# Kernel tuning notes

Measured on AMD Instinct MI355X. Metric: run time of the kernel, lower is better.

Reference implementation:

```python
import jax, jax.numpy as jnp
import numpy as np

W_BITS = 8
A_BITS = 8


def sym_quant(x, num_bits):
    # Symmetric per-last-dim abs-max quantization (SymQuantizer.forward, ndim<=3,
    # layerwise=False): s = (2^(b-1)-1)/(max|x| + 1e-6); q = round(x*s)/(s+1e-6)
    max_abs = jnp.max(jnp.abs(x), axis=-1, keepdims=True)
    s = (2.0 ** (num_bits - 1) - 1.0) / (max_abs + 1e-6)
    return jnp.round(x * s) / (s + 1e-6)


def setup_inputs() -> dict:
    key = jax.random.key(0)
    kx, kw = jax.random.split(key)
    B, S, NX, NF = 4, 2048, 1600, 6400
    x = jax.random.normal(kx, (B, S, NX), dtype=jnp.float32)
    weight = 0.02 * jax.random.normal(kw, (NX, NF), dtype=jnp.float32)  # Conv1D: [nx, nf]
    bias = jnp.zeros((NF,), dtype=jnp.float32)
    return {"x": x, "weight": weight, "bias": bias}


def reference(x, weight, bias):
    # quantize weights per-row (over nf), quantize activations per-token (over nx)
    wq = sym_quant(weight, W_BITS)
    xq = sym_quant(x, A_BITS)
    # addmm(bias, x.view(-1, nx), weight) then reshape back
    return jnp.einsum("bsx,xf->bsf", xq, wq) + bias
```

## Files before the change

### kernel.cpp

```cpp
#include <hip/hip_runtime.h>
#include <stdint.h>

typedef _Float16 f16;
typedef _Float16 f16x4 __attribute__((ext_vector_type(4)));
typedef _Float16 f16x8 __attribute__((ext_vector_type(8)));
typedef float f32x4 __attribute__((ext_vector_type(4)));

#define K_DIM 1600
#define NF_DIM 6400
#define KPAD 1664
#define NKT 26

__device__ __forceinline__ void async_copy16(const void* g, void* l) {
    __builtin_amdgcn_global_load_lds(
        (const __attribute__((address_space(1))) void*)(uintptr_t)g,
        (__attribute__((address_space(3))) void*)(uint32_t)(uintptr_t)l,
        16, 0, 0);
}

__device__ __forceinline__ float blockMax(float v, float* sm) {
#pragma unroll
    for (int off = 32; off > 0; off >>= 1)
        v = fmaxf(v, __shfl_down(v, off, 64));
    int wid = threadIdx.x >> 6, lane = threadIdx.x & 63;
    if (lane == 0) sm[wid] = v;
    __syncthreads();
    if (threadIdx.x == 0) {
        float m = sm[0];
        for (int i = 1; i < (int)(blockDim.x >> 6); ++i) m = fmaxf(m, sm[i]);
        sm[0] = m;
    }
    __syncthreads();
    return sm[0];
}

__global__ void quant_x_kernel(const float* __restrict__ x, f16* __restrict__ qx,
                               float* __restrict__ ax) {
    __shared__ float sm[4];
    size_t row = blockIdx.x;
    const float* xr = x + row * (size_t)K_DIM;
    float m = 0.f;
    const int n4 = K_DIM >> 2;
    for (int i = threadIdx.x; i < n4; i += blockDim.x) {
        float4 v = ((const float4*)xr)[i];
        m = fmaxf(fmaxf(fmaxf(fabsf(v.x), fabsf(v.y)), fmaxf(fabsf(v.z), fabsf(v.w))), m);
    }
    m = blockMax(m, sm);
    float s = 127.0f / (m + 1e-6f);
    if (threadIdx.x == 0) ax[row] = 1.0f / (s + 1e-6f);
    f16* qr = qx + row * (size_t)KPAD;
    for (int i = threadIdx.x; i < n4; i += blockDim.x) {
        float4 v = ((const float4*)xr)[i];
        f16x4 q;
        q[0] = (f16)rintf(v.x * s);
        q[1] = (f16)rintf(v.y * s);
        q[2] = (f16)rintf(v.z * s);
        q[3] = (f16)rintf(v.w * s);
        *(f16x4*)&qr[i * 4] = q;
    }
    if (threadIdx.x < 16) {
        f16x4 z = {};
        *(f16x4*)&qr[K_DIM + threadIdx.x * 4] = z;
    }
}

__global__ void wscale_kernel(const float* __restrict__ w, float* __restrict__ sw) {
    __shared__ float sm[4];
    size_t k = blockIdx.x;
    const float* wr = w + k * (size_t)NF_DIM;
    float m = 0.f;
    const int n4 = NF_DIM >> 2;
    for (int i = threadIdx.x; i < n4; i += blockDim.x) {
        float4 v = ((const float4*)wr)[i];
        m = fmaxf(fmaxf(fmaxf(fabsf(v.x), fabsf(v.y)), fmaxf(fabsf(v.z), fabsf(v.w))), m);
    }
    m = blockMax(m, sm);
    if (threadIdx.x == 0) sw[k] = 127.0f / (m + 1e-6f);
}

__global__ void wtq_kernel(const float* __restrict__ w, const float* __restrict__ sw,
                           f16* __restrict__ wqt) {
    __shared__ f16 t[64][80];
    int k0 = blockIdx.x * 64;
    int f0 = blockIdx.y * 64;
    int tid = threadIdx.x;
    if (k0 >= K_DIM) {
        int fr = tid >> 2;
        int ch = (tid & 3) << 4;
        float4 z = {};
        float4* dst = (float4*)&wqt[(size_t)(f0 + fr) * KPAD + k0 + ch];
        dst[0] = z;
        dst[1] = z;
        return;
    }
    int rr = tid >> 4;
    int cc = (tid & 15) << 2;
#pragma unroll
    for (int i = 0; i < 4; ++i) {
        int r = rr + i * 16;
        float s = sw[k0 + r];
        float inv = 1.0f / (s + 1e-6f);
        float4 v = *(const float4*)&w[(size_t)(k0 + r) * NF_DIM + f0 + cc];
        t[cc + 0][r] = (f16)(rintf(v.x * s) * inv);
        t[cc + 1][r] = (f16)(rintf(v.y * s) * inv);
        t[cc + 2][r] = (f16)(rintf(v.z * s) * inv);
        t[cc + 3][r] = (f16)(rintf(v.w * s) * inv);
    }
    __syncthreads();
    int fr = tid >> 2;
    int ch = (tid & 3) << 4;
    const float4* src = (const float4*)&t[fr][ch];
    float4* dst = (float4*)&wqt[(size_t)(f0 + fr) * KPAD + k0 + ch];
    dst[0] = src[0];
    dst[1] = src[1];
}

__global__ __launch_bounds__(512, 1) void gemm256(
    const f16* __restrict__ A,
    const f16* __restrict__ Bt,
    const float* __restrict__ ax,
    const float* __restrict__ bias,
    float* __restrict__ C, int M, int N) {
    extern __shared__ char lds[];

    const int tid = threadIdx.x;
    const int lane = tid & 63;
    const int wv = tid >> 6;
    const int wm = wv >> 2;
    const int wn = wv & 3;
    const int lr = lane & 15;
    const int lg = lane >> 4;

    const int nTn = N / 256;
    const int bid = blockIdx.x;
    const int cpx = gridDim.x >> 3;
    const int swz = (bid & 7) * cpx + (bid >> 3);
    const int tm = swz / nTn, tn = swz % nTn;
    const size_t m0 = (size_t)tm * 256, n0 = (size_t)tn * 256;

    const int srow8 = lane >> 3;
    const int sslot = (lane & 7) ^ srow8;

#define STAGE_HALF(mat, row0, kb, lhalf)                                              \
    {                                                                                 \
        _Pragma("unroll") for (int j = 0; j < 2; ++j) {                               \
            int L = (wv * 2 + j) * 1024 + lane * 16;                                  \
            int row = wv * 16 + j * 8 + srow8;                                        \
            const char* g = (const char*)((mat) + ((row0) + row) * (size_t)KPAD) +    \
                            (kb) + sslot * 16;                                        \
            async_copy16(g, (lhalf) + L);                                             \
        }                                                                             \
    }

#define STAGE_TILE(kidx, buf)                                   \
    {                                                           \
        int kb_ = (kidx) * 128;                                 \
        STAGE_HALF(A, m0, kb_, (buf));                          \
        STAGE_HALF(A, m0 + 128, kb_, (buf) + 16384);            \
        STAGE_HALF(Bt, n0, kb_, (buf) + 32768);                 \
        STAGE_HALF(Bt, n0 + 128, kb_, (buf) + 49152);           \
    }

#define LDF(base, row, s) \
    (*(const f16x8*)((base) + (row) * 128 + ((((s) ^ ((row) & 7))) << 4)))

    f32x4 acc[8][4] = {};

    STAGE_TILE(0, lds);
    STAGE_TILE(1, lds + 65536);
    asm volatile("s_waitcnt vmcnt(8)" ::: "memory");
    asm volatile("s_barrier" ::: "memory");

    for (int kt = 0; kt < NKT; ++kt) {
        char* buf = lds + (kt & 1) * 65536;
        const char* Ab = buf;
        const char* Bb = buf + 32768;
        int pf = (kt + 2 < NKT) ? kt + 2 : NKT - 1;

        f16x8 alo[4][2], ahi[4][2], bA[2][2], bB[2][2];

#pragma unroll
        for (int mi = 0; mi < 4; ++mi)
#pragma unroll
            for (int kk = 0; kk < 2; ++kk)
                alo[mi][kk] = LDF(Ab, wm * 128 + mi * 16 + lr, kk * 4 + lg);
#pragma unroll
        for (int ni = 0; ni < 2; ++ni)
#pragma unroll
            for (int kk = 0; kk < 2; ++kk)
                bA[ni][kk] = LDF(Bb, wn * 64 + ni * 16 + lr, kk * 4 + lg);
        asm volatile("s_barrier" ::: "memory");
        asm volatile("s_waitcnt lgkmcnt(0)" ::: "memory");
        __builtin_amdgcn_sched_barrier(0);
        __builtin_amdgcn_s_setprio(1);
#pragma unroll
        for (int mi = 0; mi < 4; ++mi)
#pragma unroll
            for (int ni = 0; ni < 2; ++ni)
#pragma unroll
                for (int kk = 0; kk < 2; ++kk)
                    acc[mi][ni] = __builtin_amdgcn_mfma_f32_16x16x32_f16(
                        alo[mi][kk], bA[ni][kk], acc[mi][ni], 0, 0, 0);
        __builtin_amdgcn_s_setprio(0);
        asm volatile("s_barrier" ::: "memory");

#pragma unroll
        for (int mi = 0; mi < 4; ++mi)
#pragma unroll
            for (int kk = 0; kk < 2; ++kk)
                ahi[mi][kk] = LDF(Ab, wm * 128 + 64 + mi * 16 + lr, kk * 4 + lg);
        asm volatile("s_barrier" ::: "memory");
        asm volatile("s_waitcnt lgkmcnt(0)" ::: "memory");
        __builtin_amdgcn_sched_barrier(0);
        __builtin_amdgcn_s_setprio(1);
#pragma unroll
        for (int mi = 0; mi < 4; ++mi)
#pragma unroll
            for (int ni = 0; ni < 2; ++ni)
#pragma unroll
                for (int kk = 0; kk < 2; ++kk)
                    acc[4 + mi][ni] = __builtin_amdgcn_mfma_f32_16x16x32_f16(
                        ahi[mi][kk], bA[ni][kk], acc[4 + mi][ni], 0, 0, 0);
        __builtin_amdgcn_s_setprio(0);
        asm volatile("s_barrier" ::: "memory");

#pragma unroll
        for (int ni = 0; ni < 2; ++ni)
#pragma unroll
            for (int kk = 0; kk < 2; ++kk)
                bB[ni][kk] = LDF(Bb, wn * 64 + 32 + ni * 16 + lr, kk * 4 + lg);
        asm volatile("s_barrier" ::: "memory");
        asm volatile("s_waitcnt lgkmcnt(0)" ::: "memory");
        __builtin_amdgcn_sched_barrier(0);
        __builtin_amdgcn_s_setprio(1);
#pragma unroll
        for (int mi = 0; mi < 4; ++mi)
#pragma unroll
            for (int ni = 0; ni < 2; ++ni)
#pragma unroll
                for (int kk = 0; kk < 2; ++kk)
                    acc[4 + mi][2 + ni] = __builtin_amdgcn_mfma_f32_16x16x32_f16(
                        ahi[mi][kk], bB[ni][kk], acc[4 + mi][2 + ni], 0, 0, 0);
        __builtin_amdgcn_s_setprio(0);
        asm volatile("s_barrier" ::: "memory");

        STAGE_TILE(pf, buf);
        asm volatile("s_waitcnt vmcnt(8)" ::: "memory");
        asm volatile("s_barrier" ::: "memory");
        __builtin_amdgcn_sched_barrier(0);
        __builtin_amdgcn_s_setprio(1);
#pragma unroll
        for (int mi = 0; mi < 4; ++mi)
#pragma unroll
            for (int ni = 0; ni < 2; ++ni)
#pragma unroll
                for (int kk = 0; kk < 2; ++kk)
                    acc[mi][2 + ni] = __builtin_amdgcn_mfma_f32_16x16x32_f16(
                        alo[mi][kk], bB[ni][kk], acc[mi][2 + ni], 0, 0, 0);
        __builtin_amdgcn_s_setprio(0);
        asm volatile("s_barrier" ::: "memory");
    }
    asm volatile("s_waitcnt vmcnt(0)" ::: "memory");

#pragma unroll
    for (int mi = 0; mi < 8; ++mi) {
#pragma unroll
        for (int j = 0; j < 4; ++j) {
            size_t mg = m0 + wm * 128 + mi * 16 + lg * 4 + j;
            float axv = ax[mg];
            float* crow = C + mg * (size_t)N + n0 + wn * 64;
#pragma unroll
            for (int ni = 0; ni < 4; ++ni) {
                int ng = ni * 16 + lr;
                crow[ng] = acc[mi][ni][j] * axv + bias[n0 + wn * 64 + ng];
            }
        }
    }
#undef STAGE_HALF
#undef STAGE_TILE
#undef LDF
}

extern "C" void kernel_launch(void* const* d_in, const int* in_sizes, int n_in,
                              void* d_out, int out_size, void* d_ws, size_t ws_size,
                              hipStream_t stream) {
    const float* x = (const float*)d_in[0];
    const float* w = (const float*)d_in[1];
    const float* bias = (const float*)d_in[2];
    float* out = (float*)d_out;

    const int M = in_sizes[0] / K_DIM;
    const int N = NF_DIM;

    char* ws = (char*)d_ws;
    f16* qx = (f16*)ws;
    f16* wqt = (f16*)(ws + (size_t)M * KPAD * 2);
    float* ax = (float*)(ws + (size_t)M * KPAD * 2 + (size_t)N * KPAD * 2);
    float* sw = ax + M;

    quant_x_kernel<<<M, 256, 0, stream>>>(x, qx, ax);
    wscale_kernel<<<K_DIM, 256, 0, stream>>>(w, sw);
    wtq_kernel<<<dim3(KPAD / 64, NF_DIM / 64), 256, 0, stream>>>(w, sw, wqt);

    (void)hipFuncSetAttribute((const void*)gemm256,
                              hipFuncAttributeMaxDynamicSharedMemorySize, 131072);
    gemm256<<<(M / 256) * (N / 256), 512, 131072, stream>>>(qx, wqt, ax, bias, out, M, N);
}
```

Baseline: 265.3 us.

## Stage GEMM tiles at quarter granularity interleaved with MFMA phases

Reworks the double-buffered K loop into an unrolled two-tile body. Each quarter-tile (A-lo, A-hi, B-lo, B-hi) global->LDS copy is issued as soon as its old contents have been read, instead of staging a whole tile at once. The aim is to spread memory traffic across the four MFMA phases and shorten the vmcnt waits. The price is a more intricate buffer-reuse schedule, where a misordered wait or barrier could cause read-after-overwrite hazards, and larger unrolled code.

```diff
diff --git a/kernel.cpp b/kernel.cpp
--- a/kernel.cpp
+++ b/kernel.cpp
@@ -141,124 +141,129 @@
     const int srow8 = lane >> 3;
     const int sslot = (lane & 7) ^ srow8;
 
-#define STAGE_HALF(mat, row0, kb, lhalf)                                              \
-    {                                                                                 \
-        _Pragma("unroll") for (int j = 0; j < 2; ++j) {                               \
-            int L = (wv * 2 + j) * 1024 + lane * 16;                                  \
-            int row = wv * 16 + j * 8 + srow8;                                        \
-            const char* g = (const char*)((mat) + ((row0) + row) * (size_t)KPAD) +    \
-                            (kb) + sslot * 16;                                        \
-            async_copy16(g, (lhalf) + L);                                             \
-        }                                                                             \
-    }
-
-#define STAGE_TILE(kidx, buf)                                   \
-    {                                                           \
-        int kb_ = (kidx) * 128;                                 \
-        STAGE_HALF(A, m0, kb_, (buf));                          \
-        STAGE_HALF(A, m0 + 128, kb_, (buf) + 16384);            \
-        STAGE_HALF(Bt, n0, kb_, (buf) + 32768);                 \
-        STAGE_HALF(Bt, n0 + 128, kb_, (buf) + 49152);           \
-    }
+#define STAGE_HALF(mat, grow0, kbyte, ldst)                                          \
+    {                                                                                \
+        _Pragma("unroll") for (int j_ = 0; j_ < 2; ++j_) {                           \
+            int L_ = (wv * 2 + j_) * 1024 + lane * 16;                               \
+            int row_ = wv * 16 + j_ * 8 + srow8;                                     \
+            const char* g_ = (const char*)((mat) + ((grow0) + row_) * (size_t)KPAD)  \
+                             + (kbyte) + sslot * 16;                                 \
+            async_copy16(g_, (ldst) + L_);                                           \
+        }                                                                            \
+    }
+#define ST_ALO(buf, t) STAGE_HALF(A,  m0,       (t) * 128, (buf))
+#define ST_AHI(buf, t) STAGE_HALF(A,  m0 + 128, (t) * 128, (buf) + 16384)
+#define ST_BLO(buf, t) STAGE_HALF(Bt, n0,       (t) * 128, (buf) + 32768)
+#define ST_BHI(buf, t) STAGE_HALF(Bt, n0 + 128, (t) * 128, (buf) + 49152)
 
 #define LDF(base, row, s) \
     (*(const f16x8*)((base) + (row) * 128 + ((((s) ^ ((row) & 7))) << 4)))
 
+#define RD_ALO(Ab)                                                           \
+    { _Pragma("unroll") for (int mi_ = 0; mi_ < 4; ++mi_)                    \
+      _Pragma("unroll") for (int kk_ = 0; kk_ < 2; ++kk_)                    \
+          alo[mi_][kk_] = LDF((Ab), wm * 128 + mi_ * 16 + lr, kk_ * 4 + lg); }
+#define RD_AHI(Ab)                                                           \
+    { _Pragma("unroll") for (int mi_ = 0; mi_ < 4; ++mi_)                    \
+      _Pragma("unroll") for (int kk_ = 0; kk_ < 2; ++kk_)                    \
+          ahi[mi_][kk_] = LDF((Ab), wm * 128 + 64 + mi_ * 16 + lr, kk_ * 4 + lg); }
+#define RD_BLO(Bb)                                                           \
+    { _Pragma("unroll") for (int ni_ = 0; ni_ < 2; ++ni_)                    \
+      _Pragma("unroll") for (int kk_ = 0; kk_ < 2; ++kk_)                    \
+          blo[ni_][kk_] = LDF((Bb), wn * 64 + ni_ * 16 + lr, kk_ * 4 + lg); }
+#define RD_BHI(Bb)                                                           \
+    { _Pragma("unroll") for (int ni_ = 0; ni_ < 2; ++ni_)                    \
+      _Pragma("unroll") for (int kk_ = 0; kk_ < 2; ++kk_)                    \
+          bhi[ni_][kk_] = LDF((Bb), wn * 64 + 32 + ni_ * 16 + lr, kk_ * 4 + lg); }
+
+#define BARRIER __builtin_amdgcn_s_barrier()
+#define LGKM0 asm volatile("s_waitcnt lgkmcnt(0)" ::: "memory")
+#define SB0 __builtin_amdgcn_sched_barrier(0)
+#define VM4 asm volatile("s_waitcnt vmcnt(4)" ::: "memory")
+
+#define MF(AF, BF, R0, C0)                                                        \
+    {                                                                             \
+        __builtin_amdgcn_s_setprio(1);                                            \
+        _Pragma("unroll") for (int mi_ = 0; mi_ < 4; ++mi_)                       \
+        _Pragma("unroll") for (int ni_ = 0; ni_ < 2; ++ni_)                       \
+        _Pragma("unroll") for (int kk_ = 0; kk_ < 2; ++kk_)                       \
+            acc[(R0) + mi_][(C0) + ni_] = __builtin_amdgcn_mfma_f32_16x16x32_f16( \
+                AF[mi_][kk_], BF[ni_][kk_], acc[(R0) + mi_][(C0) + ni_], 0, 0, 0);\
+        __builtin_amdgcn_s_setprio(0);                                            \
+    }
+
     f32x4 acc[8][4] = {};
-
-    STAGE_TILE(0, lds);
-    STAGE_TILE(1, lds + 65536);
-    asm volatile("s_waitcnt vmcnt(8)" ::: "memory");
-    asm volatile("s_barrier" ::: "memory");
-
-    for (int kt = 0; kt < NKT; ++kt) {
-        char* buf = lds + (kt & 1) * 65536;
-        const char* Ab = buf;
-        const char* Bb = buf + 32768;
-        int pf = (kt + 2 < NKT) ? kt + 2 : NKT - 1;
-
-        f16x8 alo[4][2], ahi[4][2], bA[2][2], bB[2][2];
-
-#pragma unroll
-        for (int mi = 0; mi < 4; ++mi)
-#pragma unroll
-            for (int kk = 0; kk < 2; ++kk)
-                alo[mi][kk] = LDF(Ab, wm * 128 + mi * 16 + lr, kk * 4 + lg);
-#pragma unroll
-        for (int ni = 0; ni < 2; ++ni)
-#pragma unroll
-            for (int kk = 0; kk < 2; ++kk)
-                bA[ni][kk] = LDF(Bb, wn * 64 + ni * 16 + lr, kk * 4 + lg);
-        asm volatile("s_barrier" ::: "memory");
-        asm volatile("s_waitcnt lgkmcnt(0)" ::: "memory");
-        __builtin_amdgcn_sched_barrier(0);
-        __builtin_amdgcn_s_setprio(1);
-#pragma unroll
-        for (int mi = 0; mi < 4; ++mi)
-#pragma unroll
-            for (int ni = 0; ni < 2; ++ni)
-#pragma unroll
-                for (int kk = 0; kk < 2; ++kk)
-                    acc[mi][ni] = __builtin_amdgcn_mfma_f32_16x16x32_f16(
-                        alo[mi][kk], bA[ni][kk], acc[mi][ni], 0, 0, 0);
-        __builtin_amdgcn_s_setprio(0);
-        asm volatile("s_barrier" ::: "memory");
-
-#pragma unroll
-        for (int mi = 0; mi < 4; ++mi)
-#pragma unroll
-            for (int kk = 0; kk < 2; ++kk)
-                ahi[mi][kk] = LDF(Ab, wm * 128 + 64 + mi * 16 + lr, kk * 4 + lg);
-        asm volatile("s_barrier" ::: "memory");
-        asm volatile("s_waitcnt lgkmcnt(0)" ::: "memory");
-        __builtin_amdgcn_sched_barrier(0);
-        __builtin_amdgcn_s_setprio(1);
-#pragma unroll
-        for (int mi = 0; mi < 4; ++mi)
-#pragma unroll
-            for (int ni = 0; ni < 2; ++ni)
-#pragma unroll
-                for (int kk = 0; kk < 2; ++kk)
-                    acc[4 + mi][ni] = __builtin_amdgcn_mfma_f32_16x16x32_f16(
-                        ahi[mi][kk], bA[ni][kk], acc[4 + mi][ni], 0, 0, 0);
-        __builtin_amdgcn_s_setprio(0);
-        asm volatile("s_barrier" ::: "memory");
-
-#pragma unroll
-        for (int ni = 0; ni < 2; ++ni)
-#pragma unroll
-            for (int kk = 0; kk < 2; ++kk)
-                bB[ni][kk] = LDF(Bb, wn * 64 + 32 + ni * 16 + lr, kk * 4 + lg);
-        asm volatile("s_barrier" ::: "memory");
-        asm volatile("s_waitcnt lgkmcnt(0)" ::: "memory");
-        __builtin_amdgcn_sched_barrier(0);
-        __builtin_amdgcn_s_setprio(1);
-#pragma unroll
-        for (int mi = 0; mi < 4; ++mi)
-#pragma unroll
-            for (int ni = 0; ni < 2; ++ni)
-#pragma unroll
-                for (int kk = 0; kk < 2; ++kk)
-                    acc[4 + mi][2 + ni] = __builtin_amdgcn_mfma_f32_16x16x32_f16(
-                        ahi[mi][kk], bB[ni][kk], acc[4 + mi][2 + ni], 0, 0, 0);
-        __builtin_amdgcn_s_setprio(0);
-        asm volatile("s_barrier" ::: "memory");
-
-        STAGE_TILE(pf, buf);
-        asm volatile("s_waitcnt vmcnt(8)" ::: "memory");
-        asm volatile("s_barrier" ::: "memory");
-        __builtin_amdgcn_sched_barrier(0);
-        __builtin_amdgcn_s_setprio(1);
-#pragma unroll
-        for (int mi = 0; mi < 4; ++mi)
-#pragma unroll
-            for (int ni = 0; ni < 2; ++ni)
-#pragma unroll
-                for (int kk = 0; kk < 2; ++kk)
-                    acc[mi][2 + ni] = __builtin_amdgcn_mfma_f32_16x16x32_f16(
-                        alo[mi][kk], bB[ni][kk], acc[mi][2 + ni], 0, 0, 0);
-        __builtin_amdgcn_s_setprio(0);
-        asm volatile("s_barrier" ::: "memory");
+    char* buf0 = lds;
+    char* buf1 = lds + 65536;
+    const char* Ab0 = buf0;
+    const char* Bb0 = buf0 + 32768;
+    const char* Ab1 = buf1;
+    const char* Bb1 = buf1 + 32768;
+
+    ST_ALO(buf0, 0);
+    ST_AHI(buf0, 0);
+    ST_BLO(buf0, 0);
+    ST_BHI(buf0, 0);
+    ST_BLO(buf1, 1);
+    ST_BHI(buf1, 1);
+    VM4;
+    BARRIER;
+
+    for (int i = 0; i < NKT / 2; ++i) {
+        const int t1s = 2 * i + 1;
+        const int tp2 = (2 * i + 2 < NKT) ? 2 * i + 2 : NKT - 1;
+        const int tp3 = (2 * i + 3 < NKT) ? 2 * i + 3 : NKT - 1;
+        f16x8 alo[4][2], ahi[4][2], blo[2][2], bhi[2][2];
+
+        RD_ALO(Ab0);
+        RD_BLO(Bb0);
+        ST_ALO(buf1, t1s);
+        BARRIER; LGKM0; SB0;
+        MF(alo, blo, 0, 0);
+        BARRIER;
+
+        RD_BHI(Bb0);
+        ST_AHI(buf1, t1s);
+        BARRIER; LGKM0; SB0;
+        MF(alo, bhi, 0, 2);
+        BARRIER;
+
+        RD_AHI(Ab0);
+        ST_BLO(buf0, tp2);
+        BARRIER; LGKM0; SB0;
+        MF(ahi, blo, 4, 0);
+        BARRIER;
+
+        ST_BHI(buf0, tp2);
+        VM4;
+        BARRIER; SB0;
+        MF(ahi, bhi, 4, 2);
+        BARRIER;
+
+        RD_ALO(Ab1);
+        RD_BLO(Bb1);
+        ST_ALO(buf0, tp2);
+        BARRIER; LGKM0; SB0;
+        MF(alo, blo, 0, 0);
+        BARRIER;
+
+        RD_BHI(Bb1);
+        ST_AHI(buf0, tp2);
+        BARRIER; LGKM0; SB0;
+        MF(alo, bhi, 0, 2);
+        BARRIER;
+
+        RD_AHI(Ab1);
+        ST_BLO(buf1, tp3);
+        BARRIER; LGKM0; SB0;
+        MF(ahi, blo, 4, 0);
+        BARRIER;
+
+        ST_BHI(buf1, tp3);
+        VM4;
+        BARRIER; SB0;
+        MF(ahi, bhi, 4, 2);
+        BARRIER;
     }
     asm volatile("s_waitcnt vmcnt(0)" ::: "memory");
 
@@ -276,9 +281,6 @@
             }
         }
     }
-#undef STAGE_HALF
-#undef STAGE_TILE
-#undef LDF
 }
 
 extern "C" void kernel_launch(void* const* d_in, const int* in_sizes, int n_in,
```

New measurement: 262.8 us. About the same (-0.9%).
